# Optimization experiments

Hardware: AMD Instinct MI355X
Metric: run time of the kernel (lower is better)

## Reference

```python
import jax, jax.numpy as jnp
import numpy as np

C_IN = 144
PC = 288           # proj_channels = 2 * in_channels
HEADS = 12
DG = 12            # deformable groups
CLIP = 2
KH = KW = 3
A = KH * KW        # samples per clip per group (attention window 3x3)
PAD = 1
MAXMAG = 10.0
B, T, H, W = 1, 1, 64, 64


def _conv2d(x, w, b, pad):
    y = jax.lax.conv_general_dilated(x, w, (1, 1), [(pad, pad), (pad, pad)],
                                     dimension_numbers=('NCHW', 'OIHW', 'NCHW'))
    return y + b[None, :, None, None]


def _lrelu(x):
    return jnp.where(x >= 0, x, 0.1 * x)


def _linear_c(x, w, b):
    # per-pixel linear on channel dim; x: (..., Cin, h, w), w: (Cin, Cout)
    return jnp.einsum('...ihw,io->...ohw', x, w) + b[:, None, None]


def _bilinear_gather(feat, py, px):
    # feat: (b, clip, g, cg, h, w); py/px: (b, clip, g, A, h, w) absolute pixel coords
    # zero padding outside image (deformable-conv sampling semantics)
    b, cl, g, cg, h, w = feat.shape
    ff = feat.reshape(b, cl, g, cg, h * w)
    y0 = jnp.floor(py)
    x0 = jnp.floor(px)
    wy1 = py - y0
    wx1 = px - x0

    def corner(yc, xc, wt):
        valid = ((yc >= 0) & (yc < h) & (xc >= 0) & (xc < w)).astype(feat.dtype)
        yi = jnp.clip(yc, 0, h - 1).astype(jnp.int32)
        xi = jnp.clip(xc, 0, w - 1).astype(jnp.int32)
        idx = (yi * w + xi).reshape(b, cl, g, 1, -1)
        gat = jnp.take_along_axis(ff, idx, axis=-1).reshape(b, cl, g, cg, *py.shape[3:])
        return gat * (wt * valid)[:, :, :, None]

    out = corner(y0, x0, (1 - wy1) * (1 - wx1))
    out = out + corner(y0, x0 + 1, (1 - wy1) * wx1)
    out = out + corner(y0 + 1, x0, wy1 * (1 - wx1))
    out = out + corner(y0 + 1, x0 + 1, wy1 * wx1)
    return out  # (b, clip, g, cg, A, h, w)


def setup_inputs() -> dict:
    key = jax.random.key(0)
    ks = jax.random.split(key, 32)
    rn = lambda i, shp, s=1.0: jax.random.normal(ks[i], shp, dtype=jnp.float32) * s
    cin_off = C_IN * (1 + CLIP) + CLIP * 2   # 436
    c_off = CLIP * DG * A * 2                # 432
    d = {
        'q': rn(0, (B, T, C_IN, H, W)),
        'k': rn(1, (B, CLIP, C_IN, H, W)),
        'v': rn(2, (B, CLIP, C_IN, H, W)),
        'vpw0': rn(3, (B, T, C_IN, H, W)),
        'vpw1': rn(4, (B, T, C_IN, H, W)),
        'flow0': rn(5, (B, T, 2, H, W), 3.0),
        'flow1': rn(6, (B, T, 2, H, W), 3.0),
        'wo1': rn(7, (64, cin_off, 1, 1), 1.0 / np.sqrt(cin_off)),
        'bo1': rn(8, (64,), 0.01),
        'wo2': rn(9, (64, 64, 3, 3), 1.0 / np.sqrt(64 * 9)),
        'bo2': rn(10, (64,), 0.01),
        'wo3': rn(11, (64, 64, 3, 3), 1.0 / np.sqrt(64 * 9)),
        'bo3': rn(12, (64,), 0.01),
        'wo4': rn(13, (64, 64, 3, 3), 1.0 / np.sqrt(64 * 9)),
        'bo4': rn(14, (64,), 0.01),
        'wo5': rn(15, (64, 64, 3, 3), 1.0 / np.sqrt(64 * 9)),
        'bo5': rn(16, (64,), 0.01),
        'wo6': rn(17, (c_off, 64, 1, 1), 0.02),
        'bo6': rn(18, (c_off,), 0.01),
        'wq': rn(19, (C_IN, PC), 1.0 / np.sqrt(C_IN)),
        'bq': rn(20, (PC,), 0.01),
        'wk': rn(21, (C_IN, PC), 1.0 / np.sqrt(C_IN)),
        'bk': rn(22, (PC,), 0.01),
        'wv': rn(23, (C_IN, PC), 1.0 / np.sqrt(C_IN)),
        'bv': rn(24, (PC,), 0.01),
        'wp': rn(25, (PC, C_IN), 1.0 / np.sqrt(PC)),
        'bp': rn(26, (C_IN,), 0.01),
        'wm1': rn(27, (C_IN, 2 * C_IN), 1.0 / np.sqrt(C_IN)),
        'bm1': rn(28, (2 * C_IN,), 0.01),
        'wm2': rn(29, (2 * C_IN, C_IN), 1.0 / np.sqrt(2 * C_IN)),
        'bm2': rn(30, (C_IN,), 0.01),
    }
    return d


def reference(q, k, v, vpw0, vpw1, flow0, flow1,
              wo1, bo1, wo2, bo2, wo3, bo3, wo4, bo4, wo5, bo5, wo6, bo6,
              wq, bq, wk, bk, wv, bv, wp, bp, wm1, bm1, wm2, bm2):
    b, t, c, h, w = q.shape  # t == 1 here so q batch b*t matches kv batch b
    bt = b * t
    # --- offset predictor: Conv3d stack with time-kernel 1 == 2D convs ---
    x = jnp.concatenate([q, vpw0, vpw1, flow0, flow1], axis=2).reshape(bt, -1, h, w)
    x = _lrelu(_conv2d(x, wo1, bo1, 0))
    x = _lrelu(_conv2d(x, wo2, bo2, 1))
    x = _lrelu(_conv2d(x, wo3, bo3, 1))
    x = _lrelu(_conv2d(x, wo4, bo4, 1))
    x = _lrelu(_conv2d(x, wo5, bo5, 1))
    off = MAXMAG * jnp.tanh(_conv2d(x, wo6, bo6, 0))  # (bt, CLIP*DG*A*2, h, w)
    # add optical flow (channel-flipped to (y, x)) to every sample offset
    fyx = flow0.reshape(bt, 2, h, w)[:, ::-1]
    off = off + jnp.tile(fyx, (1, off.shape[1] // 2, 1, 1))
    off = off.reshape(bt, CLIP, DG, A, 2, h, w)
    ar = jnp.arange(A)
    by = (ar // KW - PAD).astype(q.dtype)  # kernel base offsets (stride=1, dil=1)
    bx = (ar % KW - PAD).astype(q.dtype)
    py = off[:, :, :, :, 0] + by[None, None, None, :, None, None] \
         + jnp.arange(h, dtype=q.dtype)[:, None]
    px = off[:, :, :, :, 1] + bx[None, None, None, :, None, None] \
         + jnp.arange(w, dtype=q.dtype)
    # --- q/k/v projections ---
    hd = PC // HEADS
    qp = _linear_c(q, wq, bq).reshape(bt, HEADS, hd, h, w)
    kp = _linear_c(k, wk, bk).reshape(b, CLIP, DG, PC // DG, h, w)
    vp = _linear_c(v, wv, bv).reshape(b, CLIP, DG, PC // DG, h, w)
    # --- deformable bilinear gather (per deformable group) ---
    ksamp = _bilinear_gather(kp, py, px).reshape(bt, CLIP, HEADS, hd, A, h, w)
    vsamp = _bilinear_gather(vp, py, px).reshape(bt, CLIP, HEADS, hd, A, h, w)
    # --- attention over CLIP*A sampled locations, per pixel per head ---
    scores = jnp.einsum('bmdyx,bcmdayx->bmcayx', qp, ksamp) * (hd ** -0.5)
    attn = jax.nn.softmax(scores.reshape(bt, HEADS, CLIP * A, h, w), axis=2)
    vflat = vsamp.transpose(0, 2, 1, 4, 3, 5, 6).reshape(bt, HEADS, CLIP * A, hd, h, w)
    out = jnp.einsum('bmsyx,bmsdyx->bmdyx', attn, vflat).reshape(b, t, PC, h, w)
    # --- output projection + MLP residual ---
    o = _linear_c(out, wp, bp)
    m = _linear_c(jax.nn.gelu(_linear_c(o, wm1, bm1), approximate=False), wm2, bm2)
    return o + m
```

## Files before the change

kernel.cpp:

```cpp
#include <hip/hip_runtime.h>
#include <hip/hip_bf16.h>
#include <math.h>

typedef __hip_bfloat16 bf16;
typedef __attribute__((ext_vector_type(8))) short bf16x8v;
typedef __attribute__((ext_vector_type(4))) float f32x4v;

#define NPIX 4096

__device__ __forceinline__ float b2f(bf16 v) { return __bfloat162float(v); }
__device__ __forceinline__ unsigned short f2bu(float f) {
    bf16 h = __float2bfloat16(f);
    return *(unsigned short*)&h;
}
__device__ __forceinline__ int detect_bf16(const unsigned short* __restrict__ qraw) {
    int lane = threadIdx.x & 63;
    unsigned short u = qraw[lane * 2];
    int e = (u >> 7) & 0xFF;
    unsigned long long ball = __ballot(e >= 100 && e <= 135);
    return __popcll(ball) > 32;
}

#define OF_WO1 0
#define OF_BO1 27904
#define OF_WO2 27968
#define OF_BO2 64832
#define OF_WO3 64896
#define OF_BO3 101760
#define OF_WO4 101824
#define OF_BO4 138688
#define OF_WO5 138752
#define OF_BO5 175616
#define OF_WO6 175680
#define OF_BO6 203328
#define OF_WQ  203760
#define OF_BQ  245232
#define OF_WK  245520
#define OF_BK  286992
#define OF_WV  287280
#define OF_BV  328752
#define OF_WP  329040
#define OF_BP  370512
#define OF_WM1 370656
#define OF_BM1 412128
#define OF_WM2 412416
#define OF_BM2 453888
#define OF_FL0 454032
#define OF_FL1 462224

struct CArgs { const void* src[26]; int dstoff[26]; int n[26]; };

__global__ void misc_kernel(CArgs a, const void* __restrict__ q, const void* __restrict__ k,
                            const void* __restrict__ v, const void* __restrict__ vp0,
                            const void* __restrict__ vp1, const void* __restrict__ fl0,
                            const void* __restrict__ fl1,
                            float* __restrict__ cw, short* __restrict__ XS, short* __restrict__ X1)
{
    const int isbf = detect_bf16((const unsigned short*)q);
    const int y = blockIdx.y;
    if (y < 26) {
        const int n = a.n[y];
        float* d = cw + a.dstoff[y];
        if (isbf) {
            const bf16* s = (const bf16*)a.src[y];
            for (int i = blockIdx.x * 256 + threadIdx.x; i < n; i += 256 * 16) d[i] = b2f(s[i]);
        } else {
            const float* s = (const float*)a.src[y];
            for (int i = blockIdx.x * 256 + threadIdx.x; i < n; i += 256 * 16) d[i] = s[i];
        }
    } else if (y < 36) {
        const int job = y - 26;
        const int z = job >> 1, half = job & 1;
        const int p = blockIdx.x * 256 + threadIdx.x;
        const void* srcs[5] = { q, k, k, v, v };
        const int clips[5] = { 0, 0, 1, 0, 1 };
        const size_t co = (size_t)clips[z] * 144 * NPIX;
        short* row = XS + (size_t)z * 655360 + (size_t)p * 160;
        for (int c0 = half * 72; c0 < half * 72 + 72; c0 += 8) {
            unsigned short h[8];
            if (isbf) {
                const bf16* s = (const bf16*)srcs[z] + co;
#pragma unroll
                for (int i = 0; i < 8; ++i) h[i] = f2bu(b2f(s[(size_t)(c0 + i) * NPIX + p]));
            } else {
                const float* s = (const float*)srcs[z] + co;
#pragma unroll
                for (int i = 0; i < 8; ++i) h[i] = f2bu(s[(size_t)(c0 + i) * NPIX + p]);
            }
            uint4 u;
            u.x = (unsigned)h[0] | ((unsigned)h[1] << 16);
            u.y = (unsigned)h[2] | ((unsigned)h[3] << 16);
            u.z = (unsigned)h[4] | ((unsigned)h[5] << 16);
            u.w = (unsigned)h[6] | ((unsigned)h[7] << 16);
            *(uint4*)(row + c0) = u;
        }
        if (half == 1) {
            uint4 zz; zz.x = zz.y = zz.z = zz.w = 0u;
            *(uint4*)(row + 144) = zz;
            *(uint4*)(row + 152) = zz;
        }
    } else {
        const int sec = y - 36;
        const int p = blockIdx.x * 256 + threadIdx.x;
        short* row = X1 + (size_t)p * 448;
        if (sec < 3) {
            const void* srcs[3] = { q, vp0, vp1 };
            const int cbase = sec * 144;
            for (int c0 = 0; c0 < 144; c0 += 8) {
                unsigned short h[8];
                if (isbf) {
                    const bf16* s = (const bf16*)srcs[sec];
#pragma unroll
                    for (int i = 0; i < 8; ++i) h[i] = f2bu(b2f(s[(size_t)(c0 + i) * NPIX + p]));
                } else {
                    const float* s = (const float*)srcs[sec];
#pragma unroll
                    for (int i = 0; i < 8; ++i) h[i] = f2bu(s[(size_t)(c0 + i) * NPIX + p]);
                }
                uint4 u;
                u.x = (unsigned)h[0] | ((unsigned)h[1] << 16);
                u.y = (unsigned)h[2] | ((unsigned)h[3] << 16);
                u.z = (unsigned)h[4] | ((unsigned)h[5] << 16);
                u.w = (unsigned)h[6] | ((unsigned)h[7] << 16);
                *(uint4*)(row + cbase + c0) = u;
            }
        } else {
            unsigned short h[4];
            if (isbf) {
                const bf16* f0 = (const bf16*)fl0;
                const bf16* f1 = (const bf16*)fl1;
                h[0] = f2bu(b2f(f0[p]));
                h[1] = f2bu(b2f(f0[NPIX + p]));
                h[2] = f2bu(b2f(f1[p]));
                h[3] = f2bu(b2f(f1[NPIX + p]));
            } else {
                const float* f0 = (const float*)fl0;
                const float* f1 = (const float*)fl1;
                h[0] = f2bu(f0[p]);
                h[1] = f2bu(f0[NPIX + p]);
                h[2] = f2bu(f1[p]);
                h[3] = f2bu(f1[NPIX + p]);
            }
            uint4 u;
            u.x = (unsigned)h[0] | ((unsigned)h[1] << 16);
            u.y = (unsigned)h[2] | ((unsigned)h[3] << 16);
            u.z = 0u; u.w = 0u;
            *(uint4*)(row + 432) = u;
            uint4 zz; zz.x = zz.y = zz.z = zz.w = 0u;
            *(uint4*)(row + 440) = zz;
        }
    }
}

struct PPJob { int dstS; int Mp, Kp, kr, mr, srcof, sstride, kind; };
struct PPArgs { PPJob j[11]; };

__global__ void prepack_kernel(PPArgs pa, const float* __restrict__ cw, short* __restrict__ wsS)
{
    PPJob J = pa.j[blockIdx.y];
    const int tot = J.Mp * J.Kp;
    for (int e = blockIdx.x * 256 + threadIdx.x; e < tot; e += 256 * gridDim.x) {
        int m = e / J.Kp, kk = e - m * J.Kp;
        float v = 0.f;
        if (J.kind == 0) { if (kk < J.kr) v = cw[J.srcof + m * J.sstride + kk]; }
        else if (J.kind == 1) { if (kk < J.kr && m < J.mr) v = cw[J.srcof + kk * J.sstride + m]; }
        else { int c = kk & 63, tap = kk >> 6; if (kk < J.kr) v = cw[J.srcof + m * J.sstride + c * 9 + tap]; }
        wsS[J.dstS + e] = (short)f2bu(v);
    }
}

struct GemmDesc {
    const short* A; const short* B; const float* bias;
    void* dst; void* dst2; const unsigned short* qraw;
    int Mp, Kp, Mreal, mode, gofs, nwaves;
};
struct GemmDesc6 { GemmDesc d[6]; };

template <int TM, int TN, int BM>
__global__ __launch_bounds__(256) void gemm_kernel(GemmDesc6 gd)
{
    const GemmDesc d = gd.d[blockIdx.z];
    const int wid = blockIdx.x * 4 + (threadIdx.x >> 6);
    if (wid >= d.nwaves) return;
    const int lane = threadIdx.x & 63;
    const int tiles_m = d.Mp / (16 * TM);
    const int m0 = (wid % tiles_m) * (16 * TM);
    const int p0 = (wid / tiles_m) * (16 * TN);
    const int ar = lane & 15;
    const int kq = (lane >> 4) * 8;

    f32x4v acc[TM][TN];
#pragma unroll
    for (int i = 0; i < TM; ++i)
#pragma unroll
        for (int j = 0; j < TN; ++j) acc[i][j] = (f32x4v){0.f, 0.f, 0.f, 0.f};

    for (int k0 = 0; k0 < d.Kp; k0 += 32) {
        bf16x8v a[TM], b[TN];
#pragma unroll
        for (int i = 0; i < TM; ++i)
            a[i] = *(const bf16x8v*)(d.A + (size_t)(m0 + i * 16 + ar) * d.Kp + k0 + kq);
        if (BM == 0) {
#pragma unroll
            for (int j = 0; j < TN; ++j)
                b[j] = *(const bf16x8v*)(d.B + (size_t)(p0 + j * 16 + ar) * d.Kp + k0 + kq);
        } else {
            const int kk = k0 + kq;
            const int tap = kk >> 6, cc = kk & 63;
            const int dy = tap / 3 - 1, dx = tap % 3 - 1;
#pragma unroll
            for (int j = 0; j < TN; ++j) {
                const int pix = p0 + j * 16 + ar;
                const int yy = (pix >> 6) + dy, xx = (pix & 63) + dx;
                const bool ok = ((unsigned)yy < 64u) & ((unsigned)xx < 64u);
                const int np = min(max(yy, 0), 63) * 64 + min(max(xx, 0), 63);
                bf16x8v bv = *(const bf16x8v*)(d.B + (size_t)np * 64 + cc);
                if (!ok) bv = (bf16x8v)(short)0;
                b[j] = bv;
            }
        }
#pragma unroll
        for (int i = 0; i < TM; ++i)
#pragma unroll
            for (int j = 0; j < TN; ++j)
                acc[i][j] = __builtin_amdgcn_mfma_f32_16x16x32_bf16(a[i], b[j], acc[i][j], 0, 0, 0);
    }

    const int isbf = (d.mode == 5) ? detect_bf16(d.qraw) : 0;
#pragma unroll
    for (int i = 0; i < TM; ++i) {
#pragma unroll
        for (int j = 0; j < TN; ++j) {
            const int pcol = p0 + j * 16 + (lane & 15);
            const int mb = m0 + i * 16 + (lane >> 4) * 4;
            float vv[4];
#pragma unroll
            for (int r = 0; r < 4; ++r) {
                const int m = mb + r;
                vv[r] = acc[i][j][r];
                if (m < d.Mreal) vv[r] += d.bias[m];
            }
            if (d.mode == 0) {
#pragma unroll
                for (int r = 0; r < 4; ++r) vv[r] = (vv[r] >= 0.f) ? vv[r] : 0.1f * vv[r];
                uint2 u;
                u.x = (unsigned)f2bu(vv[0]) | ((unsigned)f2bu(vv[1]) << 16);
                u.y = (unsigned)f2bu(vv[2]) | ((unsigned)f2bu(vv[3]) << 16);
                *(uint2*)((unsigned short*)d.dst + (size_t)pcol * d.Mp + mb) = u;
            } else if (d.mode == 1) {
                const int g = mb / 24 + d.gofs;
                uint2 u;
                u.x = (unsigned)f2bu(vv[0]) | ((unsigned)f2bu(vv[1]) << 16);
                u.y = (unsigned)f2bu(vv[2]) | ((unsigned)f2bu(vv[3]) << 16);
                *(uint2*)((unsigned short*)d.dst + ((size_t)g * NPIX + pcol) * 24 + (mb % 24)) = u;
            } else if (d.mode == 3) {
                uint2 u;
                u.x = (unsigned)f2bu(vv[0]) | ((unsigned)f2bu(vv[1]) << 16);
                u.y = (unsigned)f2bu(vv[2]) | ((unsigned)f2bu(vv[3]) << 16);
                *(uint2*)((unsigned short*)d.dst + (size_t)pcol * 160 + mb) = u;
                if (mb < 144)
                    *(float4*)((float*)d.dst2 + (size_t)pcol * 144 + mb) =
                        make_float4(vv[0], vv[1], vv[2], vv[3]);
            } else if (d.mode == 4) {
#pragma unroll
                for (int r = 0; r < 4; ++r)
                    vv[r] = 0.5f * vv[r] * (1.f + erff(vv[r] * 0.70710678118654752f));
                uint2 u;
                u.x = (unsigned)f2bu(vv[0]) | ((unsigned)f2bu(vv[1]) << 16);
                u.y = (unsigned)f2bu(vv[2]) | ((unsigned)f2bu(vv[3]) << 16);
                *(uint2*)((unsigned short*)d.dst + (size_t)pcol * d.Mp + mb) = u;
            } else {
#pragma unroll
                for (int r = 0; r < 4; ++r) {
                    const int m = mb + r;
                    if (m < 144) {
                        float v = vv[r] + ((float*)d.dst2)[(size_t)pcol * 144 + m];
                        if (isbf) ((unsigned short*)d.dst)[(size_t)m * NPIX + pcol] = f2bu(v);
                        else      ((float*)d.dst)[(size_t)m * NPIX + pcol] = v;
                    }
                }
            }
        }
    }
}

__global__ __launch_bounds__(256) void conv6_kernel(const short* __restrict__ YF,
                                                    const float* __restrict__ cw,
                                                    float* __restrict__ py, float* __restrict__ px)
{
    const int p = blockIdx.x * 256 + threadIdx.x;
    const int o0 = blockIdx.y * 16;
    const uint4* yrow = (const uint4*)(YF + (size_t)p * 64);
    const float* wb = cw + OF_WO6 + o0 * 64;

    float acc[16];
#pragma unroll
    for (int j = 0; j < 16; ++j) acc[j] = cw[OF_BO6 + o0 + j];

#pragma unroll
    for (int c = 0; c < 8; ++c) {
        uint4 u = yrow[c];
        float a0 = __uint_as_float(u.x << 16);
        float a1 = __uint_as_float(u.x & 0xFFFF0000u);
        float a2 = __uint_as_float(u.y << 16);
        float a3 = __uint_as_float(u.y & 0xFFFF0000u);
        float a4 = __uint_as_float(u.z << 16);
        float a5 = __uint_as_float(u.z & 0xFFFF0000u);
        float a6 = __uint_as_float(u.w << 16);
        float a7 = __uint_as_float(u.w & 0xFFFF0000u);
#pragma unroll
        for (int j = 0; j < 16; ++j) {
            const float* wr = wb + j * 64 + c * 8;
            acc[j] += a0 * wr[0] + a1 * wr[1] + a2 * wr[2] + a3 * wr[3]
                    + a4 * wr[4] + a5 * wr[5] + a6 * wr[6] + a7 * wr[7];
        }
    }

    const float f_y = cw[OF_FL0 + NPIX + p];
    const float f_x = cw[OF_FL0 + p];
    const float yf = (float)(p >> 6), xf = (float)(p & 63);
#pragma unroll
    for (int j = 0; j < 16; ++j) {
        int o = o0 + j;
        float val = 10.f * tanhf(acc[j]);
        int s = o >> 1;
        int a_idx = s % 9;
        if ((o & 1) == 0) py[s * NPIX + p] = val + f_y + (float)(a_idx / 3 - 1) + yf;
        else              px[s * NPIX + p] = val + f_x + (float)(a_idx % 3 - 1) + xf;
    }
}

__device__ __forceinline__ float dot12(const bf16* __restrict__ row, const float* qv) {
    const uint2* s = (const uint2*)row;
    float d = 0.f;
#pragma unroll
    for (int c = 0; c < 3; ++c) {
        uint2 u = s[c];
        d += qv[c * 4 + 0] * __uint_as_float(u.x << 16);
        d += qv[c * 4 + 1] * __uint_as_float(u.x & 0xFFFF0000u);
        d += qv[c * 4 + 2] * __uint_as_float(u.y << 16);
        d += qv[c * 4 + 3] * __uint_as_float(u.y & 0xFFFF0000u);
    }
    return d;
}
__device__ __forceinline__ void acc12(float* ov, const bf16* __restrict__ row, float f) {
    const uint2* s = (const uint2*)row;
#pragma unroll
    for (int c = 0; c < 3; ++c) {
        uint2 u = s[c];
        ov[c * 4 + 0] += f * __uint_as_float(u.x << 16);
        ov[c * 4 + 1] += f * __uint_as_float(u.x & 0xFFFF0000u);
        ov[c * 4 + 2] += f * __uint_as_float(u.y << 16);
        ov[c * 4 + 3] += f * __uint_as_float(u.y & 0xFFFF0000u);
    }
}

__global__ __launch_bounds__(256) void attn_kernel(
    const bf16* __restrict__ qp, const bf16* __restrict__ kp,
    const bf16* __restrict__ vp, const float* __restrict__ py,
    const float* __restrict__ px, unsigned short* __restrict__ att)
{
    const int t = blockIdx.x * 256 + threadIdx.x;
    const int ch = t & 1;
    const int clip = (t >> 1) & 1;
    const int sh = (t >> 2) & 1;
    const int pp = t >> 3;
    const int m = pp >> 12;
    const int p = pp & 4095;

    float qv[12];
    {
        const uint2* s = (const uint2*)(qp + (size_t)(m * 4096 + p) * 24 + ch * 12);
#pragma unroll
        for (int c = 0; c < 3; ++c) {
            uint2 u = s[c];
            qv[c * 4 + 0] = __uint_as_float(u.x << 16);
            qv[c * 4 + 1] = __uint_as_float(u.x & 0xFFFF0000u);
            qv[c * 4 + 2] = __uint_as_float(u.y << 16);
            qv[c * 4 + 3] = __uint_as_float(u.y & 0xFFFF0000u);
        }
    }

    const int gidx = clip * 12 + m;
    const bf16* kb = kp + (size_t)gidx * 4096 * 24 + ch * 12;
    const bf16* vb = vp + (size_t)gidx * 4096 * 24 + ch * 12;
    const int sbase = gidx * 9;
    const int a0 = sh ? 5 : 0;
    const int na = sh ? 4 : 5;

    float e[5], fyv[5], fxv[5];
    float mx = -1e30f;
#pragma unroll
    for (int i = 0; i < 5; ++i) {
        e[i] = -1e30f; fyv[i] = 0.f; fxv[i] = 0.f;
        if (i < na) {
            const int a = a0 + i;
            const float fy = py[(sbase + a) * NPIX + p];
            const float fx = px[(sbase + a) * NPIX + p];
            fyv[i] = fy; fxv[i] = fx;
            const float y0 = floorf(fy), x0 = floorf(fx);
            const float wy = fy - y0, wx = fx - x0;
            const int iy = (int)y0, ix = (int)x0;
            const float w00 = (1.f - wy) * (1.f - wx), w01 = (1.f - wy) * wx;
            const float w10 = wy * (1.f - wx), w11 = wy * wx;
            float part = 0.f;
            if ((unsigned)iy < 64u) {
                const bf16* rr = kb + (size_t)(iy * 64) * 24;
                if ((unsigned)ix < 64u)       part += w00 * dot12(rr + ix * 24, qv);
                if ((unsigned)(ix + 1) < 64u) part += w01 * dot12(rr + (ix + 1) * 24, qv);
            }
            if ((unsigned)(iy + 1) < 64u) {
                const bf16* rr = kb + (size_t)((iy + 1) * 64) * 24;
                if ((unsigned)ix < 64u)       part += w10 * dot12(rr + ix * 24, qv);
                if ((unsigned)(ix + 1) < 64u) part += w11 * dot12(rr + (ix + 1) * 24, qv);
            }
            float full = part + __shfl_xor(part, 1, 64);
            e[i] = full * 0.20412414523193154f;
            mx = fmaxf(mx, e[i]);
        }
    }
    mx = fmaxf(mx, __shfl_xor(mx, 4, 64));
    mx = fmaxf(mx, __shfl_xor(mx, 2, 64));
    float sum = 0.f;
#pragma unroll
    for (int i = 0; i < 5; ++i) {
        if (i < na) { e[i] = __expf(e[i] - mx); sum += e[i]; }
    }
    sum += __shfl_xor(sum, 4, 64);
    sum += __shfl_xor(sum, 2, 64);
    const float inv = 1.f / sum;

    float ov[12];
#pragma unroll
    for (int j = 0; j < 12; ++j) ov[j] = 0.f;

#pragma unroll
    for (int i = 0; i < 5; ++i) {
        if (i < na) {
            const float wa = e[i] * inv;
            const float fy = fyv[i], fx = fxv[i];
            const float y0 = floorf(fy), x0 = floorf(fx);
            const float wy = fy - y0, wx = fx - x0;
            const int iy = (int)y0, ix = (int)x0;
            if ((unsigned)iy < 64u) {
                const bf16* rr = vb + (size_t)(iy * 64) * 24;
                if ((unsigned)ix < 64u)       acc12(ov, rr + ix * 24, wa * (1.f - wy) * (1.f - wx));
                if ((unsigned)(ix + 1) < 64u) acc12(ov, rr + (ix + 1) * 24, wa * (1.f - wy) * wx);
            }
            if ((unsigned)(iy + 1) < 64u) {
                const bf16* rr = vb + (size_t)((iy + 1) * 64) * 24;
                if ((unsigned)ix < 64u)       acc12(ov, rr + ix * 24, wa * wy * (1.f - wx));
                if ((unsigned)(ix + 1) < 64u) acc12(ov, rr + (ix + 1) * 24, wa * wy * wx);
            }
        }
    }
#pragma unroll
    for (int j = 0; j < 12; ++j) {
        ov[j] += __shfl_xor(ov[j], 4, 64);
        ov[j] += __shfl_xor(ov[j], 2, 64);
    }
    if (clip == 0 && sh == 0) {
        unsigned short* ab = att + (size_t)p * 288 + m * 24 + ch * 12;
#pragma unroll
        for (int c = 0; c < 3; ++c) {
            uint2 u;
            u.x = (unsigned)f2bu(ov[c * 4 + 0]) | ((unsigned)f2bu(ov[c * 4 + 1]) << 16);
            u.y = (unsigned)f2bu(ov[c * 4 + 2]) | ((unsigned)f2bu(ov[c * 4 + 3]) << 16);
            ((uint2*)ab)[c] = u;
        }
    }
}

__global__ void diag_kernel(float* __restrict__ out, int n, float v)
{
    int i = blockIdx.x * 256 + threadIdx.x;
    if (i < n) out[i] = (i == 0 ? v : 0.f);
}

extern "C" void kernel_launch(void* const* d_in, const int* in_sizes, int n_in,
                              void* d_out, int out_size, void* d_ws, size_t ws_size,
                              hipStream_t stream)
{
    const size_t REQUIRED = 75000000;
    if (ws_size < REQUIRED) {
        float code = 1000.0f + (float)(ws_size >> 20);
        diag_kernel<<<dim3((out_size + 255) / 256), 256, 0, stream>>>((float*)d_out, out_size, code);
        return;
    }

    char* W = (char*)d_ws;
    short* wsS = (short*)W;
    float* cw = (float*)(W + 64);

    short* conv1w = wsS + 1000000;
    short* conv3w[4] = { wsS + 1028672, wsS + 1065536, wsS + 1102400, wsS + 1139264 };
    short* wqb = wsS + 1176128, *wkb = wsS + 1222208, *wvb = wsS + 1268288;
    short* wpS = wsS + 1314368, *wm1S = wsS + 1360448, *wm2S = wsS + 1406528;

    short* XS = (short*)(W + 16777216);
    short* X1 = (short*)(W + 25165824);
    bf16*  QP = (bf16*)(W + 33554432);
    bf16*  KP = (bf16*)(W + 36700160);
    bf16*  VP = (bf16*)(W + 41943040);
    short* Y0 = (short*)(W + 50331648);
    short* Y1 = (short*)(W + 50855936);
    short* YF = (short*)(W + 51380224);
    float* PY = (float*)(W + 54525952);
    float* PX = (float*)(W + 58064896);
    unsigned short* ATT = (unsigned short*)(W + 62914560);
    short* OPM = (short*)(W + 67108864);
    float* O32 = (float*)(W + 68419584);
    short* M1  = (short*)(W + 71303168);

    const unsigned short* qraw = (const unsigned short*)d_in[0];

    CArgs ca;
    const int srcidx[26] = {7,8,9,10,11,12,13,14,15,16,17,18,19,20,21,22,23,24,25,26,27,28,29,30,5,6};
    const int dsto[26]   = {OF_WO1,OF_BO1,OF_WO2,OF_BO2,OF_WO3,OF_BO3,OF_WO4,OF_BO4,OF_WO5,OF_BO5,
                            OF_WO6,OF_BO6,OF_WQ,OF_BQ,OF_WK,OF_BK,OF_WV,OF_BV,OF_WP,OF_BP,
                            OF_WM1,OF_BM1,OF_WM2,OF_BM2,OF_FL0,OF_FL1};
    for (int i = 0; i < 26; ++i) {
        ca.src[i] = d_in[srcidx[i]];
        ca.dstoff[i] = dsto[i];
        ca.n[i] = in_sizes[srcidx[i]];
    }
    misc_kernel<<<dim3(16, 40), 256, 0, stream>>>(ca, d_in[0], d_in[1], d_in[2], d_in[3], d_in[4],
                                                  d_in[5], d_in[6], cw, XS, X1);

    PPArgs pp;
    pp.j[0]  = { 1000000, 64, 448, 436, 64,  OF_WO1, 436, 0 };
    pp.j[1]  = { 1028672, 64, 576, 576, 64,  OF_WO2, 576, 2 };
    pp.j[2]  = { 1065536, 64, 576, 576, 64,  OF_WO3, 576, 2 };
    pp.j[3]  = { 1102400, 64, 576, 576, 64,  OF_WO4, 576, 2 };
    pp.j[4]  = { 1139264, 64, 576, 576, 64,  OF_WO5, 576, 2 };
    pp.j[5]  = { 1176128, 288, 160, 144, 288, OF_WQ, 288, 1 };
    pp.j[6]  = { 1222208, 288, 160, 144, 288, OF_WK, 288, 1 };
    pp.j[7]  = { 1268288, 288, 160, 144, 288, OF_WV, 288, 1 };
    pp.j[8]  = { 1314368, 160, 288, 288, 144, OF_WP, 144, 1 };
    pp.j[9]  = { 1360448, 288, 160, 144, 288, OF_WM1, 288, 1 };
    pp.j[10] = { 1406528, 160, 288, 288, 144, OF_WM2, 144, 1 };
    prepack_kernel<<<dim3(64, 11), 256, 0, stream>>>(pp, cw, wsS);

    GemmDesc6 g3;
    const short* Xz[5] = { XS, XS + 655360, XS + 1310720, XS + 1966080, XS + 2621440 };
    const short* Az[5] = { wqb, wkb, wkb, wvb, wvb };
    const float* Bz[5] = { cw + OF_BQ, cw + OF_BK, cw + OF_BK, cw + OF_BV, cw + OF_BV };
    bf16* Dz[5] = { QP, KP, KP, VP, VP };
    const int Gz[5] = { 0, 0, 12, 0, 12 };
    for (int z = 0; z < 5; ++z)
        g3.d[z] = { Az[z], Xz[z], Bz[z], Dz[z], nullptr, qraw, 288, 160, 288, 1, Gz[z], 1152 };
    g3.d[5] = { conv1w, X1, cw + OF_BO1, Y0, nullptr, qraw, 64, 448, 64, 0, 0, 256 };
    gemm_kernel<2, 2, 0><<<dim3(288, 1, 6), 256, 0, stream>>>(g3);

    const float* cb[4] = { cw + OF_BO2, cw + OF_BO3, cw + OF_BO4, cw + OF_BO5 };
    short* cin[4] = { Y0, Y1, Y0, Y1 };
    short* coutp[4] = { Y1, Y0, Y1, YF };
    for (int i = 0; i < 4; ++i) {
        GemmDesc6 gc;
        gc.d[0] = { conv3w[i], cin[i], cb[i], coutp[i], nullptr, qraw, 64, 576, 64, 0, 0, 256 };
        gemm_kernel<2, 2, 1><<<dim3(64, 1, 1), 256, 0, stream>>>(gc);
    }

    conv6_kernel<<<dim3(16, 27), 256, 0, stream>>>(YF, cw, PY, PX);

    attn_kernel<<<dim3(1536), 256, 0, stream>>>(QP, KP, VP, PY, PX, ATT);

    GemmDesc6 gwp;
    gwp.d[0] = { wpS, (const short*)ATT, cw + OF_BP, OPM, O32, qraw, 160, 288, 144, 3, 0, 640 };
    gemm_kernel<2, 2, 0><<<dim3(160, 1, 1), 256, 0, stream>>>(gwp);

    GemmDesc6 gm1;
    gm1.d[0] = { wm1S, OPM, cw + OF_BM1, M1, nullptr, qraw, 288, 160, 288, 4, 0, 1152 };
    gemm_kernel<2, 2, 0><<<dim3(288, 1, 1), 256, 0, stream>>>(gm1);

    GemmDesc6 gm2;
    gm2.d[0] = { wm2S, M1, cw + OF_BM2, d_out, O32, qraw, 160, 288, 144, 5, 0, 640 };
    gemm_kernel<2, 2, 0><<<dim3(160, 1, 1), 256, 0, stream>>>(gm2);
}
```

Baseline: 304.4 us.

## Merge prepack into misc kernel, templatize GEMM K, retile convs, branchless attention gather

Folds the weight prepack into the misc conversion kernel so it reads the raw inputs directly, removing one launch and the dependency on the float staging copy. The GEMM kernel now takes K as a template parameter so the k-loop fully unrolls. The conv1 and 3x3 conv GEMMs use 1x1 wave tiles with four times as many waves to raise parallelism. The attention kernel computes clamped corner indices and validity-masked weights once per sample and reuses them for both the K and V gathers, replacing divergent branches. The cost is extra loads for padded or out-of-range samples and larger unrolled code.

Measured after the change: 279.8 us. 8.1% less time.

```diff
diff --git a/kernel.cpp b/kernel.cpp
--- a/kernel.cpp
+++ b/kernel.cpp
@@ -20,41 +20,35 @@
     unsigned long long ball = __ballot(e >= 100 && e <= 135);
     return __popcll(ball) > 32;
 }
-
-#define OF_WO1 0
-#define OF_BO1 27904
-#define OF_WO2 27968
-#define OF_BO2 64832
-#define OF_WO3 64896
-#define OF_BO3 101760
-#define OF_WO4 101824
-#define OF_BO4 138688
-#define OF_WO5 138752
-#define OF_BO5 175616
+__device__ __forceinline__ float rdval(const void* s, int idx, int isbf) {
+    return isbf ? b2f(((const bf16*)s)[idx]) : ((const float*)s)[idx];
+}
+
 #define OF_WO6 175680
 #define OF_BO6 203328
-#define OF_WQ  203760
+#define OF_BO1 27904
+#define OF_BO2 64832
+#define OF_BO3 101760
+#define OF_BO4 138688
+#define OF_BO5 175616
 #define OF_BQ  245232
-#define OF_WK  245520
 #define OF_BK  286992
-#define OF_WV  287280
 #define OF_BV  328752
-#define OF_WP  329040
 #define OF_BP  370512
-#define OF_WM1 370656
 #define OF_BM1 412128
-#define OF_WM2 412416
 #define OF_BM2 453888
 #define OF_FL0 454032
-#define OF_FL1 462224
 
 struct CArgs { const void* src[26]; int dstoff[26]; int n[26]; };
-
-__global__ void misc_kernel(CArgs a, const void* __restrict__ q, const void* __restrict__ k,
-                            const void* __restrict__ v, const void* __restrict__ vp0,
-                            const void* __restrict__ vp1, const void* __restrict__ fl0,
-                            const void* __restrict__ fl1,
-                            float* __restrict__ cw, short* __restrict__ XS, short* __restrict__ X1)
+struct PPJob { const void* src; int dstS; int Mp, Kp, kr, mr, sstride, kind; };
+struct PPArgs { PPJob j[11]; };
+
+__global__ void misc_kernel(CArgs a, PPArgs pa, const void* __restrict__ q,
+                            const void* __restrict__ k, const void* __restrict__ v,
+                            const void* __restrict__ vp0, const void* __restrict__ vp1,
+                            const void* __restrict__ fl0, const void* __restrict__ fl1,
+                            float* __restrict__ cw, short* __restrict__ XS,
+                            short* __restrict__ X1, short* __restrict__ wsS)
 {
     const int isbf = detect_bf16((const unsigned short*)q);
     const int y = blockIdx.y;
@@ -99,7 +93,7 @@
             *(uint4*)(row + 144) = zz;
             *(uint4*)(row + 152) = zz;
         }
-    } else {
+    } else if (y < 40) {
         const int sec = y - 36;
         const int p = blockIdx.x * 256 + threadIdx.x;
         short* row = X1 + (size_t)p * 448;
@@ -149,35 +143,29 @@
             uint4 zz; zz.x = zz.y = zz.z = zz.w = 0u;
             *(uint4*)(row + 440) = zz;
         }
-    }
-}
-
-struct PPJob { int dstS; int Mp, Kp, kr, mr, srcof, sstride, kind; };
-struct PPArgs { PPJob j[11]; };
-
-__global__ void prepack_kernel(PPArgs pa, const float* __restrict__ cw, short* __restrict__ wsS)
-{
-    PPJob J = pa.j[blockIdx.y];
-    const int tot = J.Mp * J.Kp;
-    for (int e = blockIdx.x * 256 + threadIdx.x; e < tot; e += 256 * gridDim.x) {
-        int m = e / J.Kp, kk = e - m * J.Kp;
-        float v = 0.f;
-        if (J.kind == 0) { if (kk < J.kr) v = cw[J.srcof + m * J.sstride + kk]; }
-        else if (J.kind == 1) { if (kk < J.kr && m < J.mr) v = cw[J.srcof + kk * J.sstride + m]; }
-        else { int c = kk & 63, tap = kk >> 6; if (kk < J.kr) v = cw[J.srcof + m * J.sstride + c * 9 + tap]; }
-        wsS[J.dstS + e] = (short)f2bu(v);
+    } else {
+        PPJob J = pa.j[y - 40];
+        const int tot = J.Mp * J.Kp;
+        for (int e = blockIdx.x * 256 + threadIdx.x; e < tot; e += 256 * 16) {
+            int m = e / J.Kp, kk = e - m * J.Kp;
+            float vv = 0.f;
+            if (J.kind == 0) { if (kk < J.kr) vv = rdval(J.src, m * J.sstride + kk, isbf); }
+            else if (J.kind == 1) { if (kk < J.kr && m < J.mr) vv = rdval(J.src, kk * J.sstride + m, isbf); }
+            else { int c = kk & 63, tap = kk >> 6; if (kk < J.kr) vv = rdval(J.src, m * J.sstride + c * 9 + tap, isbf); }
+            wsS[J.dstS + e] = (short)f2bu(vv);
+        }
     }
 }
 
 struct GemmDesc {
     const short* A; const short* B; const float* bias;
     void* dst; void* dst2; const unsigned short* qraw;
-    int Mp, Kp, Mreal, mode, gofs, nwaves;
+    int Mp, Mreal, mode, gofs, nwaves;
 };
-struct GemmDesc6 { GemmDesc d[6]; };
-
-template <int TM, int TN, int BM>
-__global__ __launch_bounds__(256) void gemm_kernel(GemmDesc6 gd)
+struct GemmDesc5 { GemmDesc d[5]; };
+
+template <int TM, int TN, int BM, int KP>
+__global__ __launch_bounds__(256) void gemm_kernel(GemmDesc5 gd)
 {
     const GemmDesc d = gd.d[blockIdx.z];
     const int wid = blockIdx.x * 4 + (threadIdx.x >> 6);
@@ -195,18 +183,19 @@
 #pragma unroll
         for (int j = 0; j < TN; ++j) acc[i][j] = (f32x4v){0.f, 0.f, 0.f, 0.f};
 
-    for (int k0 = 0; k0 < d.Kp; k0 += 32) {
+#pragma unroll
+    for (int k0 = 0; k0 < KP; k0 += 32) {
         bf16x8v a[TM], b[TN];
 #pragma unroll
         for (int i = 0; i < TM; ++i)
-            a[i] = *(const bf16x8v*)(d.A + (size_t)(m0 + i * 16 + ar) * d.Kp + k0 + kq);
+            a[i] = *(const bf16x8v*)(d.A + (size_t)(m0 + i * 16 + ar) * KP + k0 + kq);
         if (BM == 0) {
 #pragma unroll
             for (int j = 0; j < TN; ++j)
-                b[j] = *(const bf16x8v*)(d.B + (size_t)(p0 + j * 16 + ar) * d.Kp + k0 + kq);
+                b[j] = *(const bf16x8v*)(d.B + (size_t)(p0 + j * 16 + ar) * KP + k0 + kq);
         } else {
-            const int kk = k0 + kq;
-            const int tap = kk >> 6, cc = kk & 63;
+            const int tap = k0 >> 6;
+            const int cc = (k0 & 63) + kq;
             const int dy = tap / 3 - 1, dx = tap % 3 - 1;
 #pragma unroll
             for (int j = 0; j < TN; ++j) {
@@ -388,44 +377,42 @@
     const int a0 = sh ? 5 : 0;
     const int na = sh ? 4 : 5;
 
-    float e[5], fyv[5], fxv[5];
+    float e[5], w0s[5], w1s[5], w2s[5], w3s[5];
+    int n0s[5], n1s[5], n2s[5], n3s[5];
     float mx = -1e30f;
 #pragma unroll
     for (int i = 0; i < 5; ++i) {
-        e[i] = -1e30f; fyv[i] = 0.f; fxv[i] = 0.f;
-        if (i < na) {
-            const int a = a0 + i;
-            const float fy = py[(sbase + a) * NPIX + p];
-            const float fx = px[(sbase + a) * NPIX + p];
-            fyv[i] = fy; fxv[i] = fx;
-            const float y0 = floorf(fy), x0 = floorf(fx);
-            const float wy = fy - y0, wx = fx - x0;
-            const int iy = (int)y0, ix = (int)x0;
-            const float w00 = (1.f - wy) * (1.f - wx), w01 = (1.f - wy) * wx;
-            const float w10 = wy * (1.f - wx), w11 = wy * wx;
-            float part = 0.f;
-            if ((unsigned)iy < 64u) {
-                const bf16* rr = kb + (size_t)(iy * 64) * 24;
-                if ((unsigned)ix < 64u)       part += w00 * dot12(rr + ix * 24, qv);
-                if ((unsigned)(ix + 1) < 64u) part += w01 * dot12(rr + (ix + 1) * 24, qv);
-            }
-            if ((unsigned)(iy + 1) < 64u) {
-                const bf16* rr = kb + (size_t)((iy + 1) * 64) * 24;
-                if ((unsigned)ix < 64u)       part += w10 * dot12(rr + ix * 24, qv);
-                if ((unsigned)(ix + 1) < 64u) part += w11 * dot12(rr + (ix + 1) * 24, qv);
-            }
-            float full = part + __shfl_xor(part, 1, 64);
-            e[i] = full * 0.20412414523193154f;
-            mx = fmaxf(mx, e[i]);
-        }
+        const int a = min(a0 + i, 8);
+        const float fy = py[(sbase + a) * NPIX + p];
+        const float fx = px[(sbase + a) * NPIX + p];
+        const float y0f = floorf(fy), x0f = floorf(fx);
+        const float wy = fy - y0f, wx = fx - x0f;
+        const int iy = (int)y0f, ix = (int)x0f;
+        const float vy0 = ((unsigned)iy < 64u) ? 1.f : 0.f;
+        const float vy1 = ((unsigned)(iy + 1) < 64u) ? 1.f : 0.f;
+        const float vx0 = ((unsigned)ix < 64u) ? 1.f : 0.f;
+        const float vx1 = ((unsigned)(ix + 1) < 64u) ? 1.f : 0.f;
+        const int iy0 = min(max(iy, 0), 63), iy1 = min(max(iy + 1, 0), 63);
+        const int ix0 = min(max(ix, 0), 63), ix1 = min(max(ix + 1, 0), 63);
+        w0s[i] = (1.f - wy) * (1.f - wx) * vy0 * vx0;
+        w1s[i] = (1.f - wy) * wx * vy0 * vx1;
+        w2s[i] = wy * (1.f - wx) * vy1 * vx0;
+        w3s[i] = wy * wx * vy1 * vx1;
+        n0s[i] = iy0 * 64 + ix0; n1s[i] = iy0 * 64 + ix1;
+        n2s[i] = iy1 * 64 + ix0; n3s[i] = iy1 * 64 + ix1;
+        float part = w0s[i] * dot12(kb + (size_t)n0s[i] * 24, qv)
+                   + w1s[i] * dot12(kb + (size_t)n1s[i] * 24, qv)
+                   + w2s[i] * dot12(kb + (size_t)n2s[i] * 24, qv)
+                   + w3s[i] * dot12(kb + (size_t)n3s[i] * 24, qv);
+        float full = part + __shfl_xor(part, 1, 64);
+        e[i] = (i < na) ? full * 0.20412414523193154f : -1e30f;
+        mx = fmaxf(mx, e[i]);
     }
     mx = fmaxf(mx, __shfl_xor(mx, 4, 64));
     mx = fmaxf(mx, __shfl_xor(mx, 2, 64));
     float sum = 0.f;
 #pragma unroll
-    for (int i = 0; i < 5; ++i) {
-        if (i < na) { e[i] = __expf(e[i] - mx); sum += e[i]; }
-    }
+    for (int i = 0; i < 5; ++i) { e[i] = __expf(e[i] - mx); sum += e[i]; }
     sum += __shfl_xor(sum, 4, 64);
     sum += __shfl_xor(sum, 2, 64);
     const float inv = 1.f / sum;
@@ -436,23 +423,11 @@
 
 #pragma unroll
     for (int i = 0; i < 5; ++i) {
-        if (i < na) {
-            const float wa = e[i] * inv;
-            const float fy = fyv[i], fx = fxv[i];
-            const float y0 = floorf(fy), x0 = floorf(fx);
-            const float wy = fy - y0, wx = fx - x0;
-            const int iy = (int)y0, ix = (int)x0;
-            if ((unsigned)iy < 64u) {
-                const bf16* rr = vb + (size_t)(iy * 64) * 24;
-                if ((unsigned)ix < 64u)       acc12(ov, rr + ix * 24, wa * (1.f - wy) * (1.f - wx));
-                if ((unsigned)(ix + 1) < 64u) acc12(ov, rr + (ix + 1) * 24, wa * (1.f - wy) * wx);
-            }
-            if ((unsigned)(iy + 1) < 64u) {
-                const bf16* rr = vb + (size_t)((iy + 1) * 64) * 24;
-                if ((unsigned)ix < 64u)       acc12(ov, rr + ix * 24, wa * wy * (1.f - wx));
-                if ((unsigned)(ix + 1) < 64u) acc12(ov, rr + (ix + 1) * 24, wa * wy * wx);
-            }
-        }
+        const float wa = e[i] * inv;
+        acc12(ov, vb + (size_t)n0s[i] * 24, wa * w0s[i]);
+        acc12(ov, vb + (size_t)n1s[i] * 24, wa * w1s[i]);
+        acc12(ov, vb + (size_t)n2s[i] * 24, wa * w2s[i]);
+        acc12(ov, vb + (size_t)n3s[i] * 24, wa * w3s[i]);
     }
 #pragma unroll
     for (int j = 0; j < 12; ++j) {
@@ -516,64 +491,65 @@
 
     CArgs ca;
     const int srcidx[26] = {7,8,9,10,11,12,13,14,15,16,17,18,19,20,21,22,23,24,25,26,27,28,29,30,5,6};
-    const int dsto[26]   = {OF_WO1,OF_BO1,OF_WO2,OF_BO2,OF_WO3,OF_BO3,OF_WO4,OF_BO4,OF_WO5,OF_BO5,
-                            OF_WO6,OF_BO6,OF_WQ,OF_BQ,OF_WK,OF_BK,OF_WV,OF_BV,OF_WP,OF_BP,
-                            OF_WM1,OF_BM1,OF_WM2,OF_BM2,OF_FL0,OF_FL1};
+    const int dsto[26]   = {0,OF_BO1,27968,OF_BO2,64896,OF_BO3,101824,OF_BO4,138752,OF_BO5,
+                            OF_WO6,OF_BO6,203760,OF_BQ,245520,OF_BK,287280,OF_BV,329040,OF_BP,
+                            370656,OF_BM1,412416,OF_BM2,OF_FL0,462224};
     for (int i = 0; i < 26; ++i) {
         ca.src[i] = d_in[srcidx[i]];
         ca.dstoff[i] = dsto[i];
         ca.n[i] = in_sizes[srcidx[i]];
     }
-    misc_kernel<<<dim3(16, 40), 256, 0, stream>>>(ca, d_in[0], d_in[1], d_in[2], d_in[3], d_in[4],
-                                                  d_in[5], d_in[6], cw, XS, X1);
-
     PPArgs pp;
-    pp.j[0]  = { 1000000, 64, 448, 436, 64,  OF_WO1, 436, 0 };
-    pp.j[1]  = { 1028672, 64, 576, 576, 64,  OF_WO2, 576, 2 };
-    pp.j[2]  = { 1065536, 64, 576, 576, 64,  OF_WO3, 576, 2 };
-    pp.j[3]  = { 1102400, 64, 576, 576, 64,  OF_WO4, 576, 2 };
-    pp.j[4]  = { 1139264, 64, 576, 576, 64,  OF_WO5, 576, 2 };
-    pp.j[5]  = { 1176128, 288, 160, 144, 288, OF_WQ, 288, 1 };
-    pp.j[6]  = { 1222208, 288, 160, 144, 288, OF_WK, 288, 1 };
-    pp.j[7]  = { 1268288, 288, 160, 144, 288, OF_WV, 288, 1 };
-    pp.j[8]  = { 1314368, 160, 288, 288, 144, OF_WP, 144, 1 };
-    pp.j[9]  = { 1360448, 288, 160, 144, 288, OF_WM1, 288, 1 };
-    pp.j[10] = { 1406528, 160, 288, 288, 144, OF_WM2, 144, 1 };
-    prepack_kernel<<<dim3(64, 11), 256, 0, stream>>>(pp, cw, wsS);
-
-    GemmDesc6 g3;
+    pp.j[0]  = { d_in[7],  1000000, 64, 448, 436, 64,  436, 0 };
+    pp.j[1]  = { d_in[9],  1028672, 64, 576, 576, 64,  576, 2 };
+    pp.j[2]  = { d_in[11], 1065536, 64, 576, 576, 64,  576, 2 };
+    pp.j[3]  = { d_in[13], 1102400, 64, 576, 576, 64,  576, 2 };
+    pp.j[4]  = { d_in[15], 1139264, 64, 576, 576, 64,  576, 2 };
+    pp.j[5]  = { d_in[19], 1176128, 288, 160, 144, 288, 288, 1 };
+    pp.j[6]  = { d_in[21], 1222208, 288, 160, 144, 288, 288, 1 };
+    pp.j[7]  = { d_in[23], 1268288, 288, 160, 144, 288, 288, 1 };
+    pp.j[8]  = { d_in[25], 1314368, 160, 288, 288, 144, 144, 1 };
+    pp.j[9]  = { d_in[27], 1360448, 288, 160, 144, 288, 288, 1 };
+    pp.j[10] = { d_in[29], 1406528, 160, 288, 288, 144, 144, 1 };
+    misc_kernel<<<dim3(16, 51), 256, 0, stream>>>(ca, pp, d_in[0], d_in[1], d_in[2], d_in[3],
+                                                  d_in[4], d_in[5], d_in[6], cw, XS, X1, wsS);
+
+    GemmDesc5 g3;
     const short* Xz[5] = { XS, XS + 655360, XS + 1310720, XS + 1966080, XS + 2621440 };
     const short* Az[5] = { wqb, wkb, wkb, wvb, wvb };
     const float* Bz[5] = { cw + OF_BQ, cw + OF_BK, cw + OF_BK, cw + OF_BV, cw + OF_BV };
     bf16* Dz[5] = { QP, KP, KP, VP, VP };
     const int Gz[5] = { 0, 0, 12, 0, 12 };
     for (int z = 0; z < 5; ++z)
-        g3.d[z] = { Az[z], Xz[z], Bz[z], Dz[z], nullptr, qraw, 288, 160, 288, 1, Gz[z], 1152 };
-    g3.d[5] = { conv1w, X1, cw + OF_BO1, Y0, nullptr, qraw, 64, 448, 64, 0, 0, 256 };
-    gemm_kernel<2, 2, 0><<<dim3(288, 1, 6), 256, 0, stream>>>(g3);
+        g3.d[z] = { Az[z], Xz[z], Bz[z], Dz[z], nullptr, qraw, 288, 288, 1, Gz[z], 1152 };
+    gemm_kernel<2, 2, 0, 160><<<dim3(288, 1, 5), 256, 0, stream>>>(g3);
+
+    GemmDesc5 g1;
+    g1.d[0] = { conv1w, X1, cw + OF_BO1, Y0, nullptr, qraw, 64, 64, 0, 0, 1024 };
+    gemm_kernel<1, 1, 0, 448><<<dim3(256, 1, 1), 256, 0, stream>>>(g1);
 
     const float* cb[4] = { cw + OF_BO2, cw + OF_BO3, cw + OF_BO4, cw + OF_BO5 };
     short* cin[4] = { Y0, Y1, Y0, Y1 };
     short* coutp[4] = { Y1, Y0, Y1, YF };
     for (int i = 0; i < 4; ++i) {
-        GemmDesc6 gc;
-        gc.d[0] = { conv3w[i], cin[i], cb[i], coutp[i], nullptr, qraw, 64, 576, 64, 0, 0, 256 };
-        gemm_kernel<2, 2, 1><<<dim3(64, 1, 1), 256, 0, stream>>>(gc);
+        GemmDesc5 gc;
+        gc.d[0] = { conv3w[i], cin[i], cb[i], coutp[i], nullptr, qraw, 64, 64, 0, 0, 1024 };
+        gemm_kernel<1, 1, 1, 576><<<dim3(256, 1, 1), 256, 0, stream>>>(gc);
     }
 
     conv6_kernel<<<dim3(16, 27), 256, 0, stream>>>(YF, cw, PY, PX);
 
     attn_kernel<<<dim3(1536), 256, 0, stream>>>(QP, KP, VP, PY, PX, ATT);
 
-    GemmDesc6 gwp;
-    gwp.d[0] = { wpS, (const short*)ATT, cw + OF_BP, OPM, O32, qraw, 160, 288, 144, 3, 0, 640 };
-    gemm_kernel<2, 2, 0><<<dim3(160, 1, 1), 256, 0, stream>>>(gwp);
-
-    GemmDesc6 gm1;
-    gm1.d[0] = { wm1S, OPM, cw + OF_BM1, M1, nullptr, qraw, 288, 160, 288, 4, 0, 1152 };
-    gemm_kernel<2, 2, 0><<<dim3(288, 1, 1), 256, 0, stream>>>(gm1);
-
-    GemmDesc6 gm2;
-    gm2.d[0] = { wm2S, M1, cw + OF_BM2, d_out, O32, qraw, 160, 288, 144, 5, 0, 640 };
-    gemm_kernel<2, 2, 0><<<dim3(160, 1, 1), 256, 0, stream>>>(gm2);
-}
+    GemmDesc5 gwp;
+    gwp.d[0] = { wpS, (const short*)ATT, cw + OF_BP, OPM, O32, qraw, 160, 144, 3, 0, 640 };
+    gemm_kernel<2, 2, 0, 288><<<dim3(160, 1, 1), 256, 0, stream>>>(gwp);
+
+    GemmDesc5 gm1;
+    gm1.d[0] = { wm1S, OPM, cw + OF_BM1, M1, nullptr, qraw, 288, 288, 4, 0, 1152 };
+    gemm_kernel<2, 2, 0, 160><<<dim3(288, 1, 1), 256, 0, stream>>>(gm1);
+
+    GemmDesc5 gm2;
+    gm2.d[0] = { wm2S, M1, cw + OF_BM2, d_out, O32, qraw, 160, 144, 5, 0, 640 };
+    gemm_kernel<2, 2, 0, 288><<<dim3(160, 1, 1), 256, 0, stream>>>(gm2);
+}
```
